# Kernel tuning notes

Hardware: AMD Instinct MI355X
Metric: run time of the kernel (lower is better)

Reference implementation:

```python
import jax, jax.numpy as jnp
import numpy as np

NUM_DIHEDRALS = 3
# Idealized backbone geometry (picometers / radians), as in RGN/pNeRF.
BOND_LENGTHS = np.array([145.801, 152.326, 132.868], dtype=np.float32)  # N-CA, CA-C, C-N
BOND_ANGLES = np.array([2.124, 1.941, 2.028], dtype=np.float32)


def setup_inputs() -> dict:
    key = jax.random.key(0)
    num_steps, batch = 2048, 512
    flat_dihedrals = jax.random.uniform(
        key, (num_steps * batch, NUM_DIHEDRALS),
        minval=-np.pi, maxval=np.pi, dtype=jnp.float32)
    return {"flat_dihedrals": flat_dihedrals, "batch_size": batch}


def _l2_normalize(v, eps=1e-12):
    return v / jnp.sqrt(jnp.sum(v * v, axis=-1, keepdims=True) + eps)


def dihedral_to_point(dihedral):
    # dihedral: [L, B, 3] -> points in local frames: [3L, B, 3]
    r_cos_theta = np.float32(BOND_LENGTHS * np.cos(np.pi - BOND_ANGLES))  # [3]
    r_sin_theta = np.float32(BOND_LENGTHS * np.sin(np.pi - BOND_ANGLES))  # [3]
    L, B, _ = dihedral.shape
    pt_x = jnp.broadcast_to(jnp.asarray(r_cos_theta), (L, B, NUM_DIHEDRALS))
    pt_y = jnp.cos(dihedral) * r_sin_theta
    pt_z = jnp.sin(dihedral) * r_sin_theta
    point = jnp.stack([pt_x, pt_y, pt_z], axis=-1)      # [L, B, 3, 3]
    return point.reshape(L * NUM_DIHEDRALS, B, 3)       # [3L, B, 3]


def point_to_coordinate(points):
    # points: [N, B, 3]; sequential NeRF rigid-body chain extension.
    B = points.shape[1]
    init = np.array([[-np.sqrt(0.5), np.sqrt(1.5), 0.0],
                     [-np.sqrt(2.0), 0.0, 0.0],
                     [0.0, 0.0, 0.0]], dtype=np.float32)
    a = jnp.broadcast_to(jnp.asarray(init[0]), (B, 3))
    b = jnp.broadcast_to(jnp.asarray(init[1]), (B, 3))
    c = jnp.broadcast_to(jnp.asarray(init[2]), (B, 3))

    def step(carry, p):
        a, b, c = carry
        bc = _l2_normalize(c - b)                      # [B, 3]
        n = _l2_normalize(jnp.cross(b - a, bc))        # [B, 3]
        # Rotation matrix with columns [bc, n x bc, n]
        m = jnp.stack([bc, jnp.cross(n, bc), n], axis=-1)   # [B, 3, 3]
        coord = jnp.einsum('bij,bj->bi', m, p) + c          # [B, 3]
        return (b, c, coord), coord

    _, coords = jax.lax.scan(step, (a, b, c), points)
    return coords  # [N, B, 3]


def reference(flat_dihedrals, batch_size):
    num_steps = flat_dihedrals.shape[0] // batch_size
    dihedrals = flat_dihedrals.reshape(num_steps, batch_size, NUM_DIHEDRALS)
    points = dihedral_to_point(dihedrals)
    coordinates = point_to_coordinate(points)
    return coordinates
```

## Files before the change

### kernel.cpp

```cpp
#include <hip/hip_runtime.h>
#include <math.h>

#define BATCH 512
#define FRAGS 256
#define GROUP 16
#define NGRP  (FRAGS/GROUP)
#define BTILE 32
#define NTILE (BATCH/BTILE)
#define RPF   8
#define READY 0x5EADBEEF

__device__ __forceinline__ void compose(const float* A, const float* B, float* D) {
    float d[12];
    #pragma unroll
    for (int i = 0; i < 3; ++i) {
        #pragma unroll
        for (int j = 0; j < 3; ++j)
            d[i*3+j] = A[i*3+0]*B[0*3+j] + A[i*3+1]*B[1*3+j] + A[i*3+2]*B[2*3+j];
        d[9+i] = A[i*3+0]*B[9] + A[i*3+1]*B[10] + A[i*3+2]*B[11] + A[9+i];
    }
    #pragma unroll
    for (int k = 0; k < 12; ++k) D[k] = d[k];
}

__device__ __forceinline__ void frame_of(
    float ax, float ay, float az,
    float bx, float by, float bz,
    float cx, float cy, float cz,
    float* out )
{
    float bcx = cx - bx, bcy = cy - by, bcz = cz - bz;
    float inv = rsqrtf(bcx*bcx + bcy*bcy + bcz*bcz + 1e-12f);
    bcx *= inv; bcy *= inv; bcz *= inv;
    float bax = bx - ax, bay = by - ay, baz = bz - az;
    float nx = bay*bcz - baz*bcy;
    float ny = baz*bcx - bax*bcz;
    float nz = bax*bcy - bay*bcx;
    inv = rsqrtf(nx*nx + ny*ny + nz*nz + 1e-12f);
    nx *= inv; ny *= inv; nz *= inv;
    float mx = ny*bcz - nz*bcy;
    float my = nz*bcx - nx*bcz;
    float mz = nx*bcy - ny*bcx;
    out[0] = bcx; out[1] = mx; out[2] = nx;
    out[3] = bcy; out[4] = my; out[5] = ny;
    out[6] = bcz; out[7] = mz; out[8] = nz;
    out[9] = cx; out[10] = cy; out[11] = cz;
}

__device__ __forceinline__ void nerf_step(
    float ax, float ay, float az,
    float bx, float by, float bz,
    float cx, float cy, float cz,
    float px, float py, float pz,
    float& ox, float& oy, float& oz)
{
    float bcx = cx - bx, bcy = cy - by, bcz = cz - bz;
    float inv = rsqrtf(bcx*bcx + bcy*bcy + bcz*bcz + 1e-12f);
    bcx *= inv; bcy *= inv; bcz *= inv;
    float bax = bx - ax, bay = by - ay, baz = bz - az;
    float nx = bay*bcz - baz*bcy;
    float ny = baz*bcx - bax*bcz;
    float nz = bax*bcy - bay*bcx;
    inv = rsqrtf(nx*nx + ny*ny + nz*nz + 1e-12f);
    nx *= inv; ny *= inv; nz *= inv;
    float mx = ny*bcz - nz*bcy;
    float my = nz*bcx - nx*bcz;
    float mz = nx*bcy - ny*bcx;
    ox = bcx*px + mx*py + nx*pz + cx;
    oy = bcy*px + my*py + ny*pz + cy;
    oz = bcz*px + mz*py + nz*pz + cz;
}

__device__ __forceinline__ void lane_consts(int b, float* rcl, float* rsl) {
    const float PI = 3.14159265358979323846f;
    float rc[3], rs[3];
    rc[0] = 145.801f * cosf(PI - 2.124f); rs[0] = 145.801f * sinf(PI - 2.124f);
    rc[1] = 152.326f * cosf(PI - 1.941f); rs[1] = 152.326f * sinf(PI - 1.941f);
    rc[2] = 132.868f * cosf(PI - 2.028f); rs[2] = 132.868f * sinf(PI - 2.028f);
    const int d0 = b % 3, d1 = (b + 2) % 3, d2 = (b + 1) % 3;
    rcl[0] = rc[d0]; rcl[1] = rc[d1]; rcl[2] = rc[d2];
    rsl[0] = rs[d0]; rsl[1] = rs[d1]; rsl[2] = rs[d2];
}

__global__ void __launch_bounds__(GROUP * BTILE) coord_onepass(
    const float* __restrict__ dih, float* __restrict__ T,
    int* __restrict__ flags, float* __restrict__ out)
{
    const int btile = blockIdx.x & (NTILE - 1);
    const int g     = blockIdx.x >> 4;
    const int bsub  = threadIdx.x & (BTILE - 1);
    const int j     = threadIdx.x >> 5;
    const int f     = g * GROUP + j;
    const int b     = btile * BTILE + bsub;

    __shared__ float S[GROUP * BTILE * 13];
    float* Srow = &S[(size_t)threadIdx.x * 13];

    float rcl[3], rsl[3];
    lane_consts(b, rcl, rsl);

    float lx[3 * RPF], ly[3 * RPF], lz[3 * RPF];

    float ax = -0.70710678118654752f, ay = 1.22474487139158905f, az = 0.0f;
    float bx = -1.41421356237309505f, by = 0.0f, bz = 0.0f;
    float cx = 0.0f, cy = 0.0f, cz = 0.0f;

    #pragma unroll
    for (int r = 0; r < RPF; ++r) {
        int l = f * RPF + r;
        const float* src = dih + (size_t)l * (3 * BATCH) + b;
        float dd[3];
        dd[0] = src[0];
        dd[1] = src[BATCH];
        dd[2] = src[2 * BATCH];
        #pragma unroll
        for (int k = 0; k < 3; ++k) {
            float sn, cs;
            __sincosf(dd[k], &sn, &cs);
            float ox, oy, oz;
            nerf_step(ax, ay, az, bx, by, bz, cx, cy, cz,
                      rcl[k], cs * rsl[k], sn * rsl[k], ox, oy, oz);
            ax = bx; ay = by; az = bz;
            bx = cx; by = cy; bz = cz;
            cx = ox; cy = oy; cz = oz;
            lx[r * 3 + k] = ox; ly[r * 3 + k] = oy; lz[r * 3 + k] = oz;
        }
    }

    {
        float h[12];
        frame_of(ax, ay, az, bx, by, bz, cx, cy, cz, h);
        #pragma unroll
        for (int k = 0; k < 12; ++k) Srow[k] = h[k];
    }
    __syncthreads();

    float tmp[12];
    #pragma unroll
    for (int o = 1; o < GROUP; o <<= 1) {
        const bool act = (j >= o);
        if (act) compose(&S[(size_t)(threadIdx.x - o * BTILE) * 13], Srow, tmp);
        __syncthreads();
        if (act) {
            #pragma unroll
            for (int k = 0; k < 12; ++k) Srow[k] = tmp[k];
        }
        __syncthreads();
    }

    if (j == GROUP - 1) {
        #pragma unroll
        for (int k = 0; k < 12; ++k)
            __hip_atomic_store(&T[((size_t)g * 12 + k) * BATCH + b], Srow[k],
                               __ATOMIC_RELAXED, __HIP_MEMORY_SCOPE_AGENT);
    }
    __syncthreads();
    if (threadIdx.x == 0)
        __hip_atomic_store(&flags[g * NTILE + btile], READY,
                           __ATOMIC_RELEASE, __HIP_MEMORY_SCOPE_AGENT);

    if (g > 0) {
        if ((int)threadIdx.x < g) {
            while (__hip_atomic_load(&flags[threadIdx.x * NTILE + btile],
                                     __ATOMIC_ACQUIRE, __HIP_MEMORY_SCOPE_AGENT)
                   != READY) {
                __builtin_amdgcn_s_sleep(1);
            }
        }
        __syncthreads();
    }

    float G[12];
    if (g == 0) {
        G[0]=1.f; G[1]=0.f; G[2]=0.f;
        G[3]=0.f; G[4]=1.f; G[5]=0.f;
        G[6]=0.f; G[7]=0.f; G[8]=1.f;
        G[9]=0.f; G[10]=0.f; G[11]=0.f;
    } else {
        #pragma unroll
        for (int k = 0; k < 12; ++k)
            G[k] = __hip_atomic_load(&T[(size_t)k * BATCH + b],
                                     __ATOMIC_RELAXED, __HIP_MEMORY_SCOPE_AGENT);
        for (int gp = 1; gp < g; ++gp) {
            float tg[12];
            #pragma unroll
            for (int k = 0; k < 12; ++k)
                tg[k] = __hip_atomic_load(&T[((size_t)gp * 12 + k) * BATCH + b],
                                          __ATOMIC_RELAXED, __HIP_MEMORY_SCOPE_AGENT);
            compose(G, tg, G);
        }
    }
    if (j > 0) {
        compose(G, &S[(size_t)(threadIdx.x - BTILE) * 13], G);
    }

    #pragma unroll
    for (int q = 0; q < 3 * RPF; ++q) {
        float ox = lx[q], oy = ly[q], oz = lz[q];
        float gx = G[0]*ox + G[1]*oy + G[2]*oz + G[9];
        float gy = G[3]*ox + G[4]*oy + G[5]*oz + G[10];
        float gz = G[6]*ox + G[7]*oy + G[8]*oz + G[11];
        size_t n = (size_t)f * (3 * RPF) + q;
        float* dst = out + (n * BATCH + b) * 3;
        dst[0] = gx; dst[1] = gy; dst[2] = gz;
    }
}

extern "C" void kernel_launch(void* const* d_in, const int* in_sizes, int n_in,
                              void* d_out, int out_size, void* d_ws, size_t ws_size,
                              hipStream_t stream) {
    const float* dih = (const float*)d_in[0];
    float* out = (float*)d_out;
    float* T = (float*)d_ws;
    int* flags = (int*)(T + (size_t)NGRP * 12 * BATCH);

    coord_onepass<<<dim3(NGRP * NTILE), dim3(GROUP * BTILE), 0, stream>>>(
        dih, T, flags, out);
    (void)ws_size; (void)n_in; (void)out_size; (void)in_sizes;
}
```

Before: 93.94 us.

## Parallelize cross-group prefix with block scan and double-buffered intra-block scan

Replaces the serial per-thread composition of all earlier group transforms with a parallel Hillis-Steele scan over the group totals, using one lane row per prior group. The intra-block scan is double-buffered across two shared arrays, which halves the barriers per step. The flag is now published by the last row right after its store, without a block barrier, and the last group no longer writes its total. It also hoists all dihedral loads up front with nontemporal loads and uses nontemporal output stores, at the cost of more shared memory and registers.

```diff
diff --git a/kernel.cpp b/kernel.cpp
--- a/kernel.cpp
+++ b/kernel.cpp
@@ -21,6 +21,13 @@
     }
     #pragma unroll
     for (int k = 0; k < 12; ++k) D[k] = d[k];
+}
+
+__device__ __forceinline__ void set_identity(float* D) {
+    D[0]=1.f; D[1]=0.f; D[2]=0.f;
+    D[3]=0.f; D[4]=1.f; D[5]=0.f;
+    D[6]=0.f; D[7]=0.f; D[8]=1.f;
+    D[9]=0.f; D[10]=0.f; D[11]=0.f;
 }
 
 __device__ __forceinline__ void frame_of(
@@ -93,11 +100,22 @@
     const int f     = g * GROUP + j;
     const int b     = btile * BTILE + bsub;
 
-    __shared__ float S[GROUP * BTILE * 13];
-    float* Srow = &S[(size_t)threadIdx.x * 13];
+    __shared__ float BufA[GROUP * BTILE * 13];
+    __shared__ float BufB[GROUP * BTILE * 13];
+    float* rowA = &BufA[(size_t)threadIdx.x * 13];
+    float* rowB = &BufB[(size_t)threadIdx.x * 13];
 
     float rcl[3], rsl[3];
     lane_consts(b, rcl, rsl);
+
+    float dd[3 * RPF];
+    #pragma unroll
+    for (int r = 0; r < RPF; ++r) {
+        const float* src = dih + (size_t)(f * RPF + r) * (3 * BATCH) + b;
+        dd[r*3 + 0] = __builtin_nontemporal_load(src);
+        dd[r*3 + 1] = __builtin_nontemporal_load(src + BATCH);
+        dd[r*3 + 2] = __builtin_nontemporal_load(src + 2 * BATCH);
+    }
 
     float lx[3 * RPF], ly[3 * RPF], lz[3 * RPF];
 
@@ -107,91 +125,121 @@
 
     #pragma unroll
     for (int r = 0; r < RPF; ++r) {
-        int l = f * RPF + r;
-        const float* src = dih + (size_t)l * (3 * BATCH) + b;
-        float dd[3];
-        dd[0] = src[0];
-        dd[1] = src[BATCH];
-        dd[2] = src[2 * BATCH];
         #pragma unroll
         for (int k = 0; k < 3; ++k) {
             float sn, cs;
-            __sincosf(dd[k], &sn, &cs);
+            __sincosf(dd[r*3 + k], &sn, &cs);
             float ox, oy, oz;
             nerf_step(ax, ay, az, bx, by, bz, cx, cy, cz,
                       rcl[k], cs * rsl[k], sn * rsl[k], ox, oy, oz);
             ax = bx; ay = by; az = bz;
             bx = cx; by = cy; bz = cz;
             cx = ox; cy = oy; cz = oz;
-            lx[r * 3 + k] = ox; ly[r * 3 + k] = oy; lz[r * 3 + k] = oz;
-        }
-    }
-
-    {
-        float h[12];
-        frame_of(ax, ay, az, bx, by, bz, cx, cy, cz, h);
-        #pragma unroll
-        for (int k = 0; k < 12; ++k) Srow[k] = h[k];
-    }
-    __syncthreads();
-
-    float tmp[12];
-    #pragma unroll
-    for (int o = 1; o < GROUP; o <<= 1) {
-        const bool act = (j >= o);
-        if (act) compose(&S[(size_t)(threadIdx.x - o * BTILE) * 13], Srow, tmp);
-        __syncthreads();
-        if (act) {
+            lx[r*3 + k] = ox; ly[r*3 + k] = oy; lz[r*3 + k] = oz;
+        }
+    }
+
+    float cur[12];
+    frame_of(ax, ay, az, bx, by, bz, cx, cy, cz, cur);
+
+    #pragma unroll
+    for (int k = 0; k < 12; ++k) rowA[k] = cur[k];
+    __syncthreads();
+    if (j >= 1) compose(&BufA[(size_t)(threadIdx.x - 1*BTILE) * 13], cur, cur);
+
+    #pragma unroll
+    for (int k = 0; k < 12; ++k) rowB[k] = cur[k];
+    __syncthreads();
+    if (j >= 2) compose(&BufB[(size_t)(threadIdx.x - 2*BTILE) * 13], cur, cur);
+
+    #pragma unroll
+    for (int k = 0; k < 12; ++k) rowA[k] = cur[k];
+    __syncthreads();
+    if (j >= 4) compose(&BufA[(size_t)(threadIdx.x - 4*BTILE) * 13], cur, cur);
+
+    #pragma unroll
+    for (int k = 0; k < 12; ++k) rowB[k] = cur[k];
+    __syncthreads();
+    if (j >= 8) compose(&BufB[(size_t)(threadIdx.x - 8*BTILE) * 13], cur, cur);
+
+    #pragma unroll
+    for (int k = 0; k < 12; ++k) rowA[k] = cur[k];
+    __syncthreads();
+
+    float pprev[12];
+    if (j > 0) {
+        #pragma unroll
+        for (int k = 0; k < 12; ++k)
+            pprev[k] = BufA[(size_t)(threadIdx.x - BTILE) * 13 + k];
+    }
+
+    if (j == GROUP - 1 && g < NGRP - 1) {
+        #pragma unroll
+        for (int k = 0; k < 12; ++k)
+            __hip_atomic_store(&T[((size_t)g * 12 + k) * BATCH + b], cur[k],
+                               __ATOMIC_RELAXED, __HIP_MEMORY_SCOPE_AGENT);
+        if (bsub == 0)
+            __hip_atomic_store(&flags[g * NTILE + btile], READY,
+                               __ATOMIC_RELEASE, __HIP_MEMORY_SCOPE_AGENT);
+    }
+
+    float G[12];
+    if (g == 0) {
+        if (j == 0) set_identity(G);
+        else {
             #pragma unroll
-            for (int k = 0; k < 12; ++k) Srow[k] = tmp[k];
-        }
-        __syncthreads();
-    }
-
-    if (j == GROUP - 1) {
-        #pragma unroll
-        for (int k = 0; k < 12; ++k)
-            __hip_atomic_store(&T[((size_t)g * 12 + k) * BATCH + b], Srow[k],
-                               __ATOMIC_RELAXED, __HIP_MEMORY_SCOPE_AGENT);
-    }
-    __syncthreads();
-    if (threadIdx.x == 0)
-        __hip_atomic_store(&flags[g * NTILE + btile], READY,
-                           __ATOMIC_RELEASE, __HIP_MEMORY_SCOPE_AGENT);
-
-    if (g > 0) {
-        if ((int)threadIdx.x < g) {
-            while (__hip_atomic_load(&flags[threadIdx.x * NTILE + btile],
+            for (int k = 0; k < 12; ++k) G[k] = pprev[k];
+        }
+    } else {
+        float cur2[12];
+        if (j < g) {
+            while (__hip_atomic_load(&flags[j * NTILE + btile],
                                      __ATOMIC_ACQUIRE, __HIP_MEMORY_SCOPE_AGENT)
                    != READY) {
                 __builtin_amdgcn_s_sleep(1);
             }
-        }
-        __syncthreads();
-    }
-
-    float G[12];
-    if (g == 0) {
-        G[0]=1.f; G[1]=0.f; G[2]=0.f;
-        G[3]=0.f; G[4]=1.f; G[5]=0.f;
-        G[6]=0.f; G[7]=0.f; G[8]=1.f;
-        G[9]=0.f; G[10]=0.f; G[11]=0.f;
-    } else {
-        #pragma unroll
-        for (int k = 0; k < 12; ++k)
-            G[k] = __hip_atomic_load(&T[(size_t)k * BATCH + b],
-                                     __ATOMIC_RELAXED, __HIP_MEMORY_SCOPE_AGENT);
-        for (int gp = 1; gp < g; ++gp) {
-            float tg[12];
             #pragma unroll
             for (int k = 0; k < 12; ++k)
-                tg[k] = __hip_atomic_load(&T[((size_t)gp * 12 + k) * BATCH + b],
-                                          __ATOMIC_RELAXED, __HIP_MEMORY_SCOPE_AGENT);
-            compose(G, tg, G);
-        }
-    }
-    if (j > 0) {
-        compose(G, &S[(size_t)(threadIdx.x - BTILE) * 13], G);
+                cur2[k] = __hip_atomic_load(&T[((size_t)j * 12 + k) * BATCH + b],
+                                            __ATOMIC_RELAXED, __HIP_MEMORY_SCOPE_AGENT);
+        } else {
+            set_identity(cur2);
+        }
+
+        #pragma unroll
+        for (int k = 0; k < 12; ++k) rowB[k] = cur2[k];
+        __syncthreads();
+        if (j >= 1) compose(&BufB[(size_t)(threadIdx.x - 1*BTILE) * 13], cur2, cur2);
+
+        #pragma unroll
+        for (int k = 0; k < 12; ++k) rowA[k] = cur2[k];
+        __syncthreads();
+        if (j >= 2) compose(&BufA[(size_t)(threadIdx.x - 2*BTILE) * 13], cur2, cur2);
+
+        #pragma unroll
+        for (int k = 0; k < 12; ++k) rowB[k] = cur2[k];
+        __syncthreads();
+        if (j >= 4) compose(&BufB[(size_t)(threadIdx.x - 4*BTILE) * 13], cur2, cur2);
+
+        #pragma unroll
+        for (int k = 0; k < 12; ++k) rowA[k] = cur2[k];
+        __syncthreads();
+        if (j >= 8) compose(&BufA[(size_t)(threadIdx.x - 8*BTILE) * 13], cur2, cur2);
+
+        #pragma unroll
+        for (int k = 0; k < 12; ++k) rowB[k] = cur2[k];
+        __syncthreads();
+        float E[12];
+        #pragma unroll
+        for (int k = 0; k < 12; ++k)
+            E[k] = BufB[(size_t)((g - 1) * BTILE + bsub) * 13 + k];
+
+        if (j == 0) {
+            #pragma unroll
+            for (int k = 0; k < 12; ++k) G[k] = E[k];
+        } else {
+            compose(E, pprev, G);
+        }
     }
 
     #pragma unroll
@@ -202,7 +250,9 @@
         float gz = G[6]*ox + G[7]*oy + G[8]*oz + G[11];
         size_t n = (size_t)f * (3 * RPF) + q;
         float* dst = out + (n * BATCH + b) * 3;
-        dst[0] = gx; dst[1] = gy; dst[2] = gz;
+        __builtin_nontemporal_store(gx, dst + 0);
+        __builtin_nontemporal_store(gy, dst + 1);
+        __builtin_nontemporal_store(gz, dst + 2);
     }
 }
 
```

Measured after the change: 106.2 us. +13.0%, slower.
